# Performance work log

Measured on AMD Instinct MI355X. Metric: run time of the kernel, lower is better.

Reference implementation:

```python
import jax, jax.numpy as jnp
import numpy as np

B, T = 32, 2048
STATE, ACT, LAT, ENC = 128, 16, 256, 1024  # input_dim = STATE + 2*ACT = 160


def setup_inputs() -> dict:
    key = jax.random.key(0)
    ks = jax.random.split(key, 16)
    s = lambda k, shp, sc=0.05: jax.random.normal(k, shp, dtype=jnp.float32) * sc
    return {
        "padded_input": jax.random.normal(ks[0], (B, T, STATE + 2 * ACT), dtype=jnp.float32),
        "enc_w1": s(ks[1], (STATE, ENC)), "enc_b1": s(ks[2], (ENC,)),
        "enc_w2": s(ks[3], (ENC, ENC)),   "enc_b2": s(ks[4], (ENC,)),
        "enc_w3": s(ks[5], (ENC, LAT)),   "enc_b3": s(ks[6], (LAT,)),
        "a_diag": jax.random.uniform(ks[7], (LAT,), minval=-0.8, maxval=0.8, dtype=jnp.float32),
        "B_w": s(ks[8], (ACT, LAT)),
        "dec_w1": s(ks[9], (LAT, ENC)),  "dec_b1": s(ks[10], (ENC,)),
        "dec_w2": s(ks[11], (ENC, ENC)), "dec_b2": s(ks[12], (ENC,)),
        "dec_w3": s(ks[13], (ENC, STATE)), "dec_b3": s(ks[14], (STATE,)),
        "nwarmup": 4,
    }


def reference(padded_input, enc_w1, enc_b1, enc_w2, enc_b2, enc_w3, enc_b3,
              a_diag, B_w, dec_w1, dec_b1, dec_w2, dec_b2, dec_w3, dec_b3,
              nwarmup):
    # slice state / actuator channels
    x_t = padded_input[:, :, :STATE]                      # [B,T,STATE]
    u_t1 = padded_input[:, :, STATE + ACT:]               # [B,T,ACT]

    def encoder(x):
        h = jnp.tanh(x @ enc_w1 + enc_b1)
        h = jnp.tanh(h @ enc_w2 + enc_b2)
        return jnp.tanh(h @ enc_w3 + enc_b3)

    def decoder(z):
        h = jnp.tanh(z @ dec_w1 + dec_b1)
        h = jnp.tanh(h @ dec_w2 + dec_b2)
        return h @ dec_w3 + dec_b3

    z_t = encoder(x_t)                                    # [B,T,LAT]
    a = jnp.clip(a_diag, -0.95, 0.95)                     # clamped diagonal of A
    Bu = u_t1 @ B_w                                       # [B,T,LAT]

    # diagonal linear recurrence with warmup resets (reset_probability=0)
    zT = jnp.swapaxes(z_t, 0, 1)                          # [T,B,LAT]
    BuT = jnp.swapaxes(Bu, 0, 1)                          # [T,B,LAT]
    ts = jnp.arange(T)

    def step(prev, inputs):
        z, bu, t = inputs
        inp = jnp.where(t <= nwarmup, z, prev)
        out = a * inp + bu
        return out, out

    _, outs = jax.lax.scan(step, z_t[:, 0, :], (zT, BuT, ts))
    z_t1 = jnp.swapaxes(outs, 0, 1)                       # [B,T,LAT]
    return decoder(z_t1)                                  # [B,T,STATE]
```

## Files before the change

kernel.cpp:

```cpp
#include <hip/hip_runtime.h>
#include <stdint.h>
#include <type_traits>

#define B_ 32
#define T_ 2048
#define STATE_ 128
#define ACT_ 16
#define LAT_ 256
#define ENC_ 1024
#define ROWS_ (B_ * T_)
#define TENC_ 128
#define MENC_ (B_ * TENC_)
#define NCHUNK_ 64
#define LCHUNK_ 32
#define SLAB_ 32768
#define NSLAB_ 2

using bf16x8 = __attribute__((ext_vector_type(8))) short;
using f32x4  = __attribute__((ext_vector_type(4))) float;

__device__ __forceinline__ uint16_t f2bf(float f) {
  uint32_t u = __float_as_uint(f);
  u += 0x7fff + ((u >> 16) & 1);
  return (uint16_t)(u >> 16);
}

__device__ __forceinline__ float fast_tanh(float x) {
  float e = __expf(2.f * x);
  return 1.f - 2.f / (e + 1.f);
}

template <bool TANH, typename OUT_T>
__global__ __launch_bounds__(256) void gemm_bt(
    const uint16_t* __restrict__ A, const uint16_t* __restrict__ Bt,
    const float* __restrict__ bias, OUT_T* __restrict__ C,
    int M, int N, int K) {
  __shared__ uint16_t smA[128 * 64];
  __shared__ uint16_t smB[128 * 64];
  const int tid  = threadIdx.x;
  const int lane = tid & 63;
  const int wave = tid >> 6;
  const int wm = wave >> 1, wn = wave & 1;
  const int lr = lane & 15, quad = lane >> 4;
  const int m0 = blockIdx.y * 128;
  const int n0 = blockIdx.x * 128;

  const int srow = wave * 32 + (lane >> 3);
  const int sblk = lane & 7;

  f32x4 vzero = {0.f, 0.f, 0.f, 0.f};
  f32x4 acc[4][4];
#pragma unroll
  for (int i = 0; i < 4; ++i)
#pragma unroll
    for (int j = 0; j < 4; ++j) acc[i][j] = vzero;

  for (int k0 = 0; k0 < K; k0 += 64) {
#pragma unroll
    for (int i = 0; i < 4; ++i) {
      const int r  = srow + i * 8;
      const int kb = sblk ^ (r & 7);
      const uint16_t* ga = A  + (size_t)(m0 + r) * K + (k0 + kb * 8);
      const uint16_t* gb = Bt + (size_t)(n0 + r) * K + (k0 + kb * 8);
      uint16_t* la = smA + (size_t)(wave * 32 + i * 8) * 64;
      uint16_t* lb = smB + (size_t)(wave * 32 + i * 8) * 64;
      __builtin_amdgcn_global_load_lds(
          (const __attribute__((address_space(1))) void*)ga,
          (__attribute__((address_space(3))) void*)la, 16, 0, 0);
      __builtin_amdgcn_global_load_lds(
          (const __attribute__((address_space(1))) void*)gb,
          (__attribute__((address_space(3))) void*)lb, 16, 0, 0);
    }
    __syncthreads();

#pragma unroll
    for (int ks = 0; ks < 2; ++ks) {
      bf16x8 af[4], bfr[4];
#pragma unroll
      for (int mt = 0; mt < 4; ++mt) {
        const int row  = wm * 64 + mt * 16 + lr;
        const int slot = (ks * 4 + quad) ^ (lr & 7);
        af[mt] = *(const bf16x8*)(smA + row * 64 + slot * 8);
      }
#pragma unroll
      for (int nt = 0; nt < 4; ++nt) {
        const int row  = wn * 64 + nt * 16 + lr;
        const int slot = (ks * 4 + quad) ^ (lr & 7);
        bfr[nt] = *(const bf16x8*)(smB + row * 64 + slot * 8);
      }
#pragma unroll
      for (int mt = 0; mt < 4; ++mt)
#pragma unroll
        for (int nt = 0; nt < 4; ++nt)
          acc[mt][nt] = __builtin_amdgcn_mfma_f32_16x16x32_bf16(
              af[mt], bfr[nt], acc[mt][nt], 0, 0, 0);
    }
    __syncthreads();
  }

#pragma unroll
  for (int nt = 0; nt < 4; ++nt) {
    const int col = n0 + wn * 64 + nt * 16 + lr;
    const float bv = bias[col];
#pragma unroll
    for (int mt = 0; mt < 4; ++mt) {
      const int rowb = m0 + wm * 64 + mt * 16 + quad * 4;
#pragma unroll
      for (int r = 0; r < 4; ++r) {
        float v = acc[mt][nt][r] + bv;
        if (TANH) v = fast_tanh(v);
        if constexpr (std::is_same<OUT_T, uint16_t>::value)
          C[(size_t)(rowb + r) * N + col] = f2bf(v);
        else
          C[(size_t)(rowb + r) * N + col] = v;
      }
    }
  }
}

struct TArgs {
  const float* s[6];
  uint16_t* d[6];
  int R[6];
  int C[6];
};

__global__ __launch_bounds__(256) void transpose_cast(TArgs a) {
  __shared__ float tile[32][33];
  const int z = blockIdx.z;
  const float* s = a.s[z];
  uint16_t* d = a.d[z];
  const int R = a.R[z], C = a.C[z];
  const int bc = blockIdx.x * 32, br = blockIdx.y * 32;
  if (bc >= C || br >= R) return;
  const int tx = threadIdx.x & 31, ty = threadIdx.x >> 5;
#pragma unroll
  for (int i = 0; i < 32; i += 8)
    tile[ty + i][tx] = s[(size_t)(br + ty + i) * C + (bc + tx)];
  __syncthreads();
#pragma unroll
  for (int i = 0; i < 32; i += 8)
    d[(size_t)(bc + ty + i) * R + (br + tx)] = f2bf(tile[tx][ty + i]);
}

__global__ __launch_bounds__(256) void cast_x(const float* __restrict__ pin,
                                              uint16_t* __restrict__ Xc) {
  const int idx = blockIdx.x * 256 + threadIdx.x;
  const int r = idx >> 7, c = idx & 127;
  const int b = r >> 7, t = r & 127;
  Xc[idx] = f2bf(pin[((size_t)b * T_ + t) * 160 + c]);
}

__global__ __launch_bounds__(256) void bu_kernel(const float* __restrict__ pin,
                                                 const float* __restrict__ Bw,
                                                 float* __restrict__ Bu) {
  const int r = blockIdx.x;
  const int l = threadIdx.x;
  const float* u = pin + (size_t)r * 160 + 144;
  float s = 0.f;
#pragma unroll
  for (int k = 0; k < 16; ++k) s += u[k] * Bw[k * LAT_ + l];
  Bu[(size_t)r * LAT_ + l] = s;
}

__device__ __forceinline__ float clip_a(const float* a_diag, int l) {
  return fminf(fmaxf(a_diag[l], -0.95f), 0.95f);
}

__global__ __launch_bounds__(256) void rec_pass1(
    const float* __restrict__ Zc, const float* __restrict__ Bu,
    const float* __restrict__ a_diag, const int* __restrict__ nwp,
    float* __restrict__ F) {
  const int l = threadIdx.x, c = blockIdx.x, b = blockIdx.y;
  const int nw = *nwp;
  const float a = clip_a(a_diag, l);
  float s = (c == 0) ? Zc[(size_t)b * TENC_ * LAT_ + l] : 0.f;
  const int t0 = c * LCHUNK_;
  for (int j = 0; j < LCHUNK_; ++j) {
    const int t = t0 + j;
    float inp;
    if (t <= nw) {
      const int tt = t < TENC_ ? t : TENC_ - 1;
      inp = Zc[((size_t)b * TENC_ + tt) * LAT_ + l];
    } else {
      inp = s;
    }
    s = a * inp + Bu[((size_t)b * T_ + t) * LAT_ + l];
  }
  F[((size_t)c * B_ + b) * LAT_ + l] = s;
}

__global__ __launch_bounds__(256) void rec_pass2(
    const float* __restrict__ Zc, const float* __restrict__ F,
    const float* __restrict__ a_diag, const int* __restrict__ nwp,
    float* __restrict__ I) {
  const int l = threadIdx.x, b = blockIdx.x;
  const int nw = *nwp;
  const float a = clip_a(a_diag, l);
  float aL = a;
#pragma unroll
  for (int i = 0; i < 5; ++i) aL *= aL;
  float s = Zc[(size_t)b * TENC_ * LAT_ + l];
  I[(size_t)b * LAT_ + l] = s;
  for (int c = 1; c < NCHUNK_; ++c) {
    const float Fp = F[((size_t)(c - 1) * B_ + b) * LAT_ + l];
    const bool exact = ((c - 1) == 0) || (nw >= (c - 1) * LCHUNK_);
    s = exact ? Fp : (aL * s + Fp);
    I[((size_t)c * B_ + b) * LAT_ + l] = s;
  }
}

__global__ __launch_bounds__(256) void rec_pass3(
    const float* __restrict__ Zc, const float* __restrict__ Bu,
    const float* __restrict__ a_diag, const int* __restrict__ nwp,
    const float* __restrict__ I, uint16_t* __restrict__ Zp) {
  const int l = threadIdx.x, c = blockIdx.x, b = blockIdx.y;
  const int nw = *nwp;
  const float a = clip_a(a_diag, l);
  float s = I[((size_t)c * B_ + b) * LAT_ + l];
  const int t0 = c * LCHUNK_;
  for (int j = 0; j < LCHUNK_; ++j) {
    const int t = t0 + j;
    float inp;
    if (t <= nw) {
      const int tt = t < TENC_ ? t : TENC_ - 1;
      inp = Zc[((size_t)b * TENC_ + tt) * LAT_ + l];
    } else {
      inp = s;
    }
    s = a * inp + Bu[((size_t)b * T_ + t) * LAT_ + l];
    Zp[((size_t)b * T_ + t) * LAT_ + l] = f2bf(s);
  }
}

extern "C" void kernel_launch(void* const* d_in, const int* in_sizes, int n_in,
                              void* d_out, int out_size, void* d_ws,
                              size_t ws_size, hipStream_t stream) {
  const float* pin = (const float*)d_in[0];
  const float* ew1 = (const float*)d_in[1];
  const float* eb1 = (const float*)d_in[2];
  const float* ew2 = (const float*)d_in[3];
  const float* eb2 = (const float*)d_in[4];
  const float* ew3 = (const float*)d_in[5];
  const float* eb3 = (const float*)d_in[6];
  const float* adg = (const float*)d_in[7];
  const float* Bw  = (const float*)d_in[8];
  const float* dw1 = (const float*)d_in[9];
  const float* db1 = (const float*)d_in[10];
  const float* dw2 = (const float*)d_in[11];
  const float* db2 = (const float*)d_in[12];
  const float* dw3 = (const float*)d_in[13];
  const float* db3 = (const float*)d_in[14];
  const int* nwp   = (const int*)d_in[15];
  float* out = (float*)d_out;

  uint8_t* ws = (uint8_t*)d_ws;
  size_t off = 0;
  auto alloc = [&](size_t b) -> void* {
    void* p = ws + off;
    off += (b + 255) & ~(size_t)255;
    return p;
  };
  uint16_t* W1t = (uint16_t*)alloc((size_t)ENC_ * STATE_ * 2);
  uint16_t* W2t = (uint16_t*)alloc((size_t)ENC_ * ENC_ * 2);
  uint16_t* W3t = (uint16_t*)alloc((size_t)LAT_ * ENC_ * 2);
  uint16_t* D1t = (uint16_t*)alloc((size_t)ENC_ * LAT_ * 2);
  uint16_t* D2t = (uint16_t*)alloc((size_t)ENC_ * ENC_ * 2);
  uint16_t* D3t = (uint16_t*)alloc((size_t)STATE_ * ENC_ * 2);
  uint16_t* Xc  = (uint16_t*)alloc((size_t)MENC_ * STATE_ * 2);
  float* Zc = (float*)alloc((size_t)MENC_ * LAT_ * 4);
  float* F  = (float*)alloc((size_t)NCHUNK_ * B_ * LAT_ * 4);
  float* I  = (float*)alloc((size_t)NCHUNK_ * B_ * LAT_ * 4);
  uint16_t* Zp = (uint16_t*)alloc((size_t)ROWS_ * LAT_ * 2);
  uint16_t* G1 = (uint16_t*)alloc((size_t)SLAB_ * ENC_ * 2);
  uint16_t* G2 = (uint16_t*)alloc((size_t)SLAB_ * ENC_ * 2);
  uint16_t* H1c = G1;
  uint16_t* H2c = G1 + (size_t)MENC_ * ENC_;
  float* Bu = (float*)G2;

  if (ws_size < off) return;

  TArgs ta;
  ta.s[0] = ew1; ta.d[0] = W1t; ta.R[0] = STATE_; ta.C[0] = ENC_;
  ta.s[1] = ew2; ta.d[1] = W2t; ta.R[1] = ENC_;   ta.C[1] = ENC_;
  ta.s[2] = ew3; ta.d[2] = W3t; ta.R[2] = ENC_;   ta.C[2] = LAT_;
  ta.s[3] = dw1; ta.d[3] = D1t; ta.R[3] = LAT_;   ta.C[3] = ENC_;
  ta.s[4] = dw2; ta.d[4] = D2t; ta.R[4] = ENC_;   ta.C[4] = ENC_;
  ta.s[5] = dw3; ta.d[5] = D3t; ta.R[5] = ENC_;   ta.C[5] = STATE_;
  transpose_cast<<<dim3(32, 32, 6), 256, 0, stream>>>(ta);

  cast_x<<<dim3((MENC_ * STATE_) / 256), 256, 0, stream>>>(pin, Xc);

  gemm_bt<true, uint16_t><<<dim3(ENC_ / 128, MENC_ / 128), 256, 0, stream>>>(
      Xc, W1t, eb1, H1c, MENC_, ENC_, STATE_);
  gemm_bt<true, uint16_t><<<dim3(ENC_ / 128, MENC_ / 128), 256, 0, stream>>>(
      H1c, W2t, eb2, H2c, MENC_, ENC_, ENC_);
  gemm_bt<true, float><<<dim3(LAT_ / 128, MENC_ / 128), 256, 0, stream>>>(
      H2c, W3t, eb3, Zc, MENC_, LAT_, ENC_);

  bu_kernel<<<dim3(ROWS_), 256, 0, stream>>>(pin, Bw, Bu);
  rec_pass1<<<dim3(NCHUNK_, B_), 256, 0, stream>>>(Zc, Bu, adg, nwp, F);
  rec_pass2<<<dim3(B_), 256, 0, stream>>>(Zc, F, adg, nwp, I);
  rec_pass3<<<dim3(NCHUNK_, B_), 256, 0, stream>>>(Zc, Bu, adg, nwp, I, Zp);

  for (int s = 0; s < NSLAB_; ++s) {
    const uint16_t* Zs = Zp + (size_t)s * SLAB_ * LAT_;
    float* Os = out + (size_t)s * SLAB_ * STATE_;
    gemm_bt<true, uint16_t><<<dim3(ENC_ / 128, SLAB_ / 128), 256, 0, stream>>>(
        Zs, D1t, db1, G1, SLAB_, ENC_, LAT_);
    gemm_bt<true, uint16_t><<<dim3(ENC_ / 128, SLAB_ / 128), 256, 0, stream>>>(
        G1, D2t, db2, G2, SLAB_, ENC_, ENC_);
    gemm_bt<false, float><<<dim3(STATE_ / 128, SLAB_ / 128), 256, 0, stream>>>(
        G2, D3t, db3, Os, SLAB_, STATE_, ENC_);
  }
}
```

Baseline: 597.4 us.

## Fuse Bu projection into recurrence passes and add XCD-aware GEMM tile remap

```diff
diff --git a/kernel.cpp b/kernel.cpp
--- a/kernel.cpp
+++ b/kernel.cpp
@@ -42,8 +42,22 @@
   const int wave = tid >> 6;
   const int wm = wave >> 1, wn = wave & 1;
   const int lr = lane & 15, quad = lane >> 4;
-  const int m0 = blockIdx.y * 128;
-  const int n0 = blockIdx.x * 128;
+
+  const int gx = gridDim.x, gy = gridDim.y;
+  int bm, bn;
+  if (((gy & 7) == 0) && ((gx & (gx - 1)) == 0)) {
+    const int lin  = blockIdx.y * gx + blockIdx.x;
+    const int xcd  = lin & 7;
+    const int slot = lin >> 3;
+    const int lgx  = 31 - __clz(gx);
+    bn = slot & (gx - 1);
+    bm = ((slot >> lgx) << 3) + xcd;
+  } else {
+    bm = blockIdx.y;
+    bn = blockIdx.x;
+  }
+  const int m0 = bm * 128;
+  const int n0 = bn * 128;
 
   const int srow = wave * 32 + (lane >> 3);
   const int sblk = lane & 7;
@@ -151,31 +165,29 @@
   Xc[idx] = f2bf(pin[((size_t)b * T_ + t) * 160 + c]);
 }
 
-__global__ __launch_bounds__(256) void bu_kernel(const float* __restrict__ pin,
-                                                 const float* __restrict__ Bw,
-                                                 float* __restrict__ Bu) {
-  const int r = blockIdx.x;
-  const int l = threadIdx.x;
-  const float* u = pin + (size_t)r * 160 + 144;
-  float s = 0.f;
-#pragma unroll
-  for (int k = 0; k < 16; ++k) s += u[k] * Bw[k * LAT_ + l];
-  Bu[(size_t)r * LAT_ + l] = s;
-}
-
 __device__ __forceinline__ float clip_a(const float* a_diag, int l) {
   return fminf(fmaxf(a_diag[l], -0.95f), 0.95f);
 }
 
 __global__ __launch_bounds__(256) void rec_pass1(
-    const float* __restrict__ Zc, const float* __restrict__ Bu,
-    const float* __restrict__ a_diag, const int* __restrict__ nwp,
-    float* __restrict__ F) {
+    const float* __restrict__ Zc, const float* __restrict__ pin,
+    const float* __restrict__ Bw, const float* __restrict__ a_diag,
+    const int* __restrict__ nwp, float* __restrict__ F) {
+  __shared__ float uS[LCHUNK_][ACT_];
   const int l = threadIdx.x, c = blockIdx.x, b = blockIdx.y;
   const int nw = *nwp;
   const float a = clip_a(a_diag, l);
+  const int t0 = c * LCHUNK_;
+  for (int idx = threadIdx.x; idx < LCHUNK_ * ACT_; idx += 256) {
+    const int j = idx >> 4, k = idx & 15;
+    uS[j][k] = pin[((size_t)b * T_ + (t0 + j)) * 160 + 144 + k];
+  }
+  float bw[ACT_];
+#pragma unroll
+  for (int k = 0; k < ACT_; ++k) bw[k] = Bw[k * LAT_ + l];
+  __syncthreads();
+
   float s = (c == 0) ? Zc[(size_t)b * TENC_ * LAT_ + l] : 0.f;
-  const int t0 = c * LCHUNK_;
   for (int j = 0; j < LCHUNK_; ++j) {
     const int t = t0 + j;
     float inp;
@@ -185,7 +197,10 @@
     } else {
       inp = s;
     }
-    s = a * inp + Bu[((size_t)b * T_ + t) * LAT_ + l];
+    float bu = 0.f;
+#pragma unroll
+    for (int k = 0; k < ACT_; ++k) bu += uS[j][k] * bw[k];
+    s = a * inp + bu;
   }
   F[((size_t)c * B_ + b) * LAT_ + l] = s;
 }
@@ -211,14 +226,25 @@
 }
 
 __global__ __launch_bounds__(256) void rec_pass3(
-    const float* __restrict__ Zc, const float* __restrict__ Bu,
-    const float* __restrict__ a_diag, const int* __restrict__ nwp,
-    const float* __restrict__ I, uint16_t* __restrict__ Zp) {
+    const float* __restrict__ Zc, const float* __restrict__ pin,
+    const float* __restrict__ Bw, const float* __restrict__ a_diag,
+    const int* __restrict__ nwp, const float* __restrict__ I,
+    uint16_t* __restrict__ Zp) {
+  __shared__ float uS[LCHUNK_][ACT_];
   const int l = threadIdx.x, c = blockIdx.x, b = blockIdx.y;
   const int nw = *nwp;
   const float a = clip_a(a_diag, l);
+  const int t0 = c * LCHUNK_;
+  for (int idx = threadIdx.x; idx < LCHUNK_ * ACT_; idx += 256) {
+    const int j = idx >> 4, k = idx & 15;
+    uS[j][k] = pin[((size_t)b * T_ + (t0 + j)) * 160 + 144 + k];
+  }
+  float bw[ACT_];
+#pragma unroll
+  for (int k = 0; k < ACT_; ++k) bw[k] = Bw[k * LAT_ + l];
+  __syncthreads();
+
   float s = I[((size_t)c * B_ + b) * LAT_ + l];
-  const int t0 = c * LCHUNK_;
   for (int j = 0; j < LCHUNK_; ++j) {
     const int t = t0 + j;
     float inp;
@@ -228,7 +254,10 @@
     } else {
       inp = s;
     }
-    s = a * inp + Bu[((size_t)b * T_ + t) * LAT_ + l];
+    float bu = 0.f;
+#pragma unroll
+    for (int k = 0; k < ACT_; ++k) bu += uS[j][k] * bw[k];
+    s = a * inp + bu;
     Zp[((size_t)b * T_ + t) * LAT_ + l] = f2bf(s);
   }
 }
@@ -276,7 +305,6 @@
   uint16_t* G2 = (uint16_t*)alloc((size_t)SLAB_ * ENC_ * 2);
   uint16_t* H1c = G1;
   uint16_t* H2c = G1 + (size_t)MENC_ * ENC_;
-  float* Bu = (float*)G2;
 
   if (ws_size < off) return;
 
@@ -298,10 +326,10 @@
   gemm_bt<true, float><<<dim3(LAT_ / 128, MENC_ / 128), 256, 0, stream>>>(
       H2c, W3t, eb3, Zc, MENC_, LAT_, ENC_);
 
-  bu_kernel<<<dim3(ROWS_), 256, 0, stream>>>(pin, Bw, Bu);
-  rec_pass1<<<dim3(NCHUNK_, B_), 256, 0, stream>>>(Zc, Bu, adg, nwp, F);
+  rec_pass1<<<dim3(NCHUNK_, B_), 256, 0, stream>>>(Zc, pin, Bw, adg, nwp, F);
   rec_pass2<<<dim3(B_), 256, 0, stream>>>(Zc, F, adg, nwp, I);
-  rec_pass3<<<dim3(NCHUNK_, B_), 256, 0, stream>>>(Zc, Bu, adg, nwp, I, Zp);
+  rec_pass3<<<dim3(NCHUNK_, B_), 256, 0, stream>>>(Zc, pin, Bw, adg, nwp, I,
+                                                   Zp);
 
   for (int s = 0; s < NSLAB_; ++s) {
     const uint16_t* Zs = Zp + (size_t)s * SLAB_ * LAT_;
```

New measurement: 534.9 us. 1.12x faster.
